# Performance work log

Hardware: AMD Instinct MI355X
Metric: run time of the kernel (lower is better)

## Reference

```python
import jax, jax.numpy as jnp
import numpy as np

H, C, HID, NLAYERS, B = 4, 32, 128, 3, 2048
EPS = 1e-5


def _gat_layer(x, src, dst, n, W, b, a_src, a_dst):
    # x: [N, HID]; W: [HID, H*C]; a_src/a_dst: [H, C]
    h = (x @ W).reshape(n, H, C)                      # [N,H,C]
    s_src = jnp.einsum('nhc,hc->nh', h, a_src)        # [N,H]
    s_dst = jnp.einsum('nhc,hc->nh', h, a_dst)
    e = jax.nn.leaky_relu(s_src[src] + s_dst[dst], 0.2)   # [E,H]
    m = jax.ops.segment_max(e, dst, num_segments=n)
    p = jnp.exp(e - m[dst])
    z = jax.ops.segment_sum(p, dst, num_segments=n)
    alpha = p / z[dst]                                 # scatter-softmax over in-edges
    msg = h[src] * alpha[:, :, None]                   # [E,H,C]
    out = jax.ops.segment_sum(msg, dst, num_segments=n)
    return out.reshape(n, H * C) + b


def _layernorm(x, g, bta):
    mu = jnp.mean(x, axis=-1, keepdims=True)
    var = jnp.mean(jnp.square(x - mu), axis=-1, keepdims=True)
    return (x - mu) * jax.lax.rsqrt(var + EPS) * g + bta


def _encode(x, edge_index, batch, W_in, b_in, Wg, bg, att_src, att_dst, ln_gamma, ln_beta):
    n = x.shape[0]
    # add self loops (PyG GATConv default)
    loops = jnp.arange(n, dtype=edge_index.dtype)
    src = jnp.concatenate([edge_index[0], loops])
    dst = jnp.concatenate([edge_index[1], loops])
    h = jax.nn.relu(x @ W_in + b_in)
    for i in range(NLAYERS):
        res = h
        h = _gat_layer(h, src, dst, n, Wg[i], bg[i], att_src[i], att_dst[i])
        h = _layernorm(h, ln_gamma[i], ln_beta[i])
        h = jax.nn.relu(h)
        h = h + res
    # global mean pool
    sums = jax.ops.segment_sum(h, batch, num_segments=B)
    cnt = jax.ops.segment_sum(jnp.ones((n,), h.dtype), batch, num_segments=B)
    return sums / jnp.maximum(cnt, 1.0)[:, None]


def setup_inputs() -> dict:
    key = jax.random.key(0)
    ks = jax.random.split(key, 24)
    Nt, Et, Np, Ep, D = 131072, 2097152, 24576, 196608, 480
    inp = {}
    inp['tcr_x'] = jax.random.normal(ks[0], (Nt, D), jnp.float32)
    inp['tcr_edge_index'] = jax.random.randint(ks[1], (2, Et), 0, Nt)
    inp['tcr_batch'] = jnp.sort(jax.random.randint(ks[2], (Nt,), 0, B))
    inp['pep_x'] = jax.random.normal(ks[3], (Np, D), jnp.float32)
    inp['pep_edge_index'] = jax.random.randint(ks[4], (2, Ep), 0, Np)
    inp['pep_batch'] = jnp.sort(jax.random.randint(ks[5], (Np,), 0, B))
    s_in = 1.0 / np.sqrt(D)
    inp['W_in'] = jax.random.normal(ks[6], (D, HID), jnp.float32) * s_in
    inp['b_in'] = jnp.zeros((HID,), jnp.float32)
    s_h = 1.0 / np.sqrt(HID)
    inp['Wg'] = jax.random.normal(ks[7], (NLAYERS, HID, H * C), jnp.float32) * s_h
    inp['bg'] = jnp.zeros((NLAYERS, HID), jnp.float32)
    inp['att_src'] = jax.random.normal(ks[8], (NLAYERS, H, C), jnp.float32) * (1.0 / np.sqrt(C))
    inp['att_dst'] = jax.random.normal(ks[9], (NLAYERS, H, C), jnp.float32) * (1.0 / np.sqrt(C))
    inp['ln_gamma'] = jnp.ones((NLAYERS, HID), jnp.float32)
    inp['ln_beta'] = jnp.zeros((NLAYERS, HID), jnp.float32)
    inp['Wc1'] = jax.random.normal(ks[10], (2 * HID, HID), jnp.float32) * (1.0 / np.sqrt(2 * HID))
    inp['bc1'] = jnp.zeros((HID,), jnp.float32)
    inp['Wc2'] = jax.random.normal(ks[11], (HID, HID // 2), jnp.float32) * s_h
    inp['bc2'] = jnp.zeros((HID // 2,), jnp.float32)
    inp['Wc3'] = jax.random.normal(ks[12], (HID // 2, 1), jnp.float32) * (1.0 / np.sqrt(HID // 2))
    inp['bc3'] = jnp.zeros((1,), jnp.float32)
    return inp


def reference(tcr_x, tcr_edge_index, tcr_batch, pep_x, pep_edge_index, pep_batch,
              W_in, b_in, Wg, bg, att_src, att_dst, ln_gamma, ln_beta,
              Wc1, bc1, Wc2, bc2, Wc3, bc3):
    tcr = _encode(tcr_x, tcr_edge_index, tcr_batch, W_in, b_in, Wg, bg, att_src, att_dst, ln_gamma, ln_beta)
    pep = _encode(pep_x, pep_edge_index, pep_batch, W_in, b_in, Wg, bg, att_src, att_dst, ln_gamma, ln_beta)
    z = jnp.concatenate([tcr, pep], axis=1)            # [B, 256]
    z = jax.nn.relu(z @ Wc1 + bc1)
    z = jax.nn.relu(z @ Wc2 + bc2)
    return jax.nn.sigmoid(z @ Wc3 + bc3)               # [B, 1]
```

## Files before the change

kernel.cpp:

```cpp
#include <hip/hip_runtime.h>
#include <hip/hip_fp16.h>
#include <math.h>

#define NHEAD   4
#define CDIM    32
#define HIDDIM  128
#define NLAYERS 3
#define DIN     480
#define LN_EPS  1e-5f
#define NSPLIT  4

typedef _Float16 f16x8 __attribute__((ext_vector_type(8)));
typedef float    f32x4 __attribute__((ext_vector_type(4)));
typedef int      int4u __attribute__((ext_vector_type(4), aligned(4)));

__global__ void hist_kernel(const int* __restrict__ tei, const int* __restrict__ pei,
                            int* __restrict__ deg, int Et, int Ep, int Nt, int N) {
    int i = blockIdx.x * 256 + threadIdx.x;
    int tot = Et + Ep + N;
    if (i >= tot) return;
    int d;
    if (i < Et)            d = tei[Et + i];
    else if (i < Et + Ep)  d = pei[Ep + (i - Et)] + Nt;
    else                   d = i - Et - Ep;
    atomicAdd(&deg[d], 1);
}

__global__ __launch_bounds__(256) void fill_kernel(const int* __restrict__ tei,
                                                   const int* __restrict__ pei,
                                                   int* __restrict__ cursor,
                                                   int* __restrict__ col,
                                                   int Et, int Ep, int Nt, int N,
                                                   float oscale) {
    int oid    = blockIdx.x & (NSPLIT - 1);
    int chunk  = blockIdx.x / NSPLIT;
    int nchunk = gridDim.x / NSPLIT;
    int tot = Et + Ep + N;
    int per = (tot + nchunk - 1) / nchunk;
    int e0 = chunk * per;
    int e1 = min(e0 + per, tot);
    for (int i = e0 + (int)threadIdx.x; i < e1; i += 256) {
        int d;
        bool self = false;
        if (i < Et)           d = tei[Et + i];
        else if (i < Et + Ep) d = pei[Ep + (i - Et)] + Nt;
        else                { d = i - Et - Ep; self = true; }
        int owner = (int)((float)d * oscale);
        owner = owner > NSPLIT - 1 ? NSPLIT - 1 : owner;
        if (owner != oid) continue;
        int s;
        if (self)        s = d;
        else if (i < Et) s = tei[i];
        else             s = pei[i - Et] + Nt;
        int pos = atomicAdd(&cursor[d], 1);
        col[pos] = s;
    }
}

__global__ __launch_bounds__(256) void scan_reduce(const int* __restrict__ deg,
                                                   int* __restrict__ part, int N) {
    __shared__ int sm[256];
    int t = threadIdx.x;
    int base = blockIdx.x * 1024 + t * 4;
    int4 v = make_int4(0, 0, 0, 0);
    if (base + 3 < N) v = *(const int4*)(deg + base);
    else if (base < N) {
        v.x = deg[base];
        if (base + 1 < N) v.y = deg[base + 1];
        if (base + 2 < N) v.z = deg[base + 2];
    }
    sm[t] = v.x + v.y + v.z + v.w;
    __syncthreads();
    for (int off = 128; off >= 1; off >>= 1) {
        if (t < off) sm[t] += sm[t + off];
        __syncthreads();
    }
    if (t == 0) part[blockIdx.x] = sm[0];
}

__global__ __launch_bounds__(256) void scan_partials(int* __restrict__ part,
                                                     int* __restrict__ rowptr,
                                                     int npart, int N) {
    __shared__ int sm[256];
    int t = threadIdx.x;
    sm[t] = (t < npart) ? part[t] : 0;
    __syncthreads();
    for (int off = 1; off < 256; off <<= 1) {
        int u = (t >= off) ? sm[t - off] : 0;
        __syncthreads();
        sm[t] += u;
        __syncthreads();
    }
    if (t < npart) part[t] = (t == 0) ? 0 : sm[t - 1];
    if (t == 0) rowptr[N] = sm[255];
}

__global__ __launch_bounds__(256) void scan_final(const int* __restrict__ deg,
                                                  const int* __restrict__ part,
                                                  int* __restrict__ rowptr,
                                                  int* __restrict__ cursor, int N) {
    __shared__ int sm[256];
    int t = threadIdx.x;
    int base = blockIdx.x * 1024 + t * 4;
    int4 v = make_int4(0, 0, 0, 0);
    if (base + 3 < N) v = *(const int4*)(deg + base);
    else if (base < N) {
        v.x = deg[base];
        if (base + 1 < N) v.y = deg[base + 1];
        if (base + 2 < N) v.z = deg[base + 2];
    }
    sm[t] = v.x + v.y + v.z + v.w;
    __syncthreads();
    for (int off = 1; off < 256; off <<= 1) {
        int u = (t >= off) ? sm[t - off] : 0;
        __syncthreads();
        sm[t] += u;
        __syncthreads();
    }
    int run = ((t == 0) ? 0 : sm[t - 1]) + part[blockIdx.x];
    if (base < N)     { rowptr[base]     = run; cursor[base]     = run; run += v.x; }
    if (base + 1 < N) { rowptr[base + 1] = run; cursor[base + 1] = run; run += v.y; }
    if (base + 2 < N) { rowptr[base + 2] = run; cursor[base + 2] = run; run += v.z; }
    if (base + 3 < N) { rowptr[base + 3] = run; cursor[base + 3] = run; }
}

__global__ void transpose_w(const float* __restrict__ W, _Float16* __restrict__ Wt,
                            int K) {
    int idx = blockIdx.x * 256 + threadIdx.x;
    if (idx >= K * 128) return;
    int n = idx / K, k = idx - n * K;
    Wt[idx] = (_Float16)W[(size_t)k * 128 + n];
}

#define ASTRIDE 40

template<int OUT_F16>
__global__ __launch_bounds__(256) void mfma_gemm(const float* __restrict__ A,
                                                 const _Float16* __restrict__ Wt,
                                                 const float* __restrict__ bias,
                                                 void* __restrict__ Cout,
                                                 int K) {
    __shared__ _Float16 As[64 * ASTRIDE];
    __shared__ _Float16 Ws[128 * ASTRIDE];
    const int tid  = threadIdx.x;
    const int bn   = blockIdx.x * 64;
    const int wave = tid >> 6, lane = tid & 63;
    const int lm   = lane & 15, q = lane >> 4;

    f32x4 acc[8];
#pragma unroll
    for (int i = 0; i < 8; ++i) acc[i] = (f32x4){0.f, 0.f, 0.f, 0.f};

    for (int kt = 0; kt < K; kt += 32) {
#pragma unroll
        for (int p = 0; p < 2; ++p) {
            int f  = p * 256 + tid;
            int r  = f >> 3;
            int c4 = (f & 7) * 4;
            float4 v = *(const float4*)(A + (size_t)(bn + r) * K + kt + c4);
            _Float16* d = &As[r * ASTRIDE + c4];
            d[0] = (_Float16)v.x; d[1] = (_Float16)v.y;
            d[2] = (_Float16)v.z; d[3] = (_Float16)v.w;
        }
#pragma unroll
        for (int p = 0; p < 2; ++p) {
            int f   = p * 256 + tid;
            int n   = f >> 2;
            int seg = (f & 3) * 8;
            *(float4*)(&Ws[n * ASTRIDE + seg]) =
                *(const float4*)(Wt + (size_t)n * K + kt + seg);
        }
        __syncthreads();
        f16x8 af = *(const f16x8*)(&As[(wave * 16 + lm) * ASTRIDE + q * 8]);
#pragma unroll
        for (int nt = 0; nt < 8; ++nt) {
            f16x8 bf = *(const f16x8*)(&Ws[(nt * 16 + lm) * ASTRIDE + q * 8]);
            acc[nt] = __builtin_amdgcn_mfma_f32_16x16x32_f16(af, bf, acc[nt], 0, 0, 0);
        }
        __syncthreads();
    }

    const int row0 = bn + wave * 16 + q * 4;
    if (OUT_F16) {
        _Float16* C = (_Float16*)Cout;
#pragma unroll
        for (int nt = 0; nt < 8; ++nt) {
            int c = nt * 16 + lm;
#pragma unroll
            for (int i = 0; i < 4; ++i)
                C[(size_t)(row0 + i) * 128 + c] = (_Float16)acc[nt][i];
        }
    } else {
        float* C = (float*)Cout;
#pragma unroll
        for (int nt = 0; nt < 8; ++nt) {
            int c = nt * 16 + lm;
            float bv = bias[c];
#pragma unroll
            for (int i = 0; i < 4; ++i)
                C[(size_t)(row0 + i) * 128 + c] = fmaxf(acc[nt][i] + bv, 0.f);
        }
    }
}

__global__ __launch_bounds__(256) void scores_kernel(const __half2* __restrict__ h2v,
                                                     const float* __restrict__ a_src,
                                                     const float* __restrict__ a_dst,
                                                     float* __restrict__ ssrc,
                                                     float* __restrict__ sdst, int N) {
    int wave = threadIdx.x >> 6, lane = threadIdx.x & 63;
    int n = blockIdx.x * 4 + wave;
    if (n >= N) return;
    int c = lane * 2, h = lane >> 4, t = lane & 15;
    float2 v = __half22float2(h2v[(size_t)n * 64 + lane]);
    float2 as = *(const float2*)(a_src + c);
    float2 ad = *(const float2*)(a_dst + c);
    float ps = v.x * as.x + v.y * as.y;
    float pd = v.x * ad.x + v.y * ad.y;
#pragma unroll
    for (int k = 1; k < 16; k <<= 1) {
        ps += __shfl_xor(ps, k, 16);
        pd += __shfl_xor(pd, k, 16);
    }
    if (t == 0) {
        ssrc[n * 4 + h] = ps;
        sdst[n * 4 + h] = pd;
    }
}

__global__ __launch_bounds__(256) void gather_kernel(const f16x8* __restrict__ h2v,
                                                     const float* __restrict__ ssrc,
                                                     const float* __restrict__ sdst,
                                                     const int* __restrict__ rowptr,
                                                     const int* __restrict__ col,
                                                     const float* __restrict__ bg,
                                                     const float* __restrict__ gamma,
                                                     const float* __restrict__ beta,
                                                     float* __restrict__ hio, int N) {
    int wave = threadIdx.x >> 6, lane = threadIdx.x & 63;
    int g = lane >> 4, t = lane & 15;
    int n = blockIdx.x * 16 + wave * 4 + g;
    bool valid = n < N;
    int nn = valid ? n : 0;
    int head = t >> 2;
    int beg = rowptr[nn];
    int end = valid ? rowptr[nn + 1] : beg;
    float sd = sdst[nn * 4 + head];

    float m = -1e30f, z = 0.f;
    float a[8];
#pragma unroll
    for (int k = 0; k < 8; ++k) a[k] = 0.f;

    int j = beg;
    for (; j + 3 < end; j += 4) {
        int4u cv = *(const int4u*)(col + j);
        int s0 = cv.x, s1 = cv.y, s2 = cv.z, s3 = cv.w;
        float e0 = ssrc[s0 * 4 + head] + sd;
        float e1 = ssrc[s1 * 4 + head] + sd;
        float e2 = ssrc[s2 * 4 + head] + sd;
        float e3 = ssrc[s3 * 4 + head] + sd;
        f16x8 v0 = h2v[(size_t)s0 * 16 + t];
        f16x8 v1 = h2v[(size_t)s1 * 16 + t];
        f16x8 v2 = h2v[(size_t)s2 * 16 + t];
        f16x8 v3 = h2v[(size_t)s3 * 16 + t];
        e0 = fmaxf(e0, 0.2f * e0);
        e1 = fmaxf(e1, 0.2f * e1);
        e2 = fmaxf(e2, 0.2f * e2);
        e3 = fmaxf(e3, 0.2f * e3);
        float nm = fmaxf(fmaxf(fmaxf(e0, e1), fmaxf(e2, e3)), m);
        float r  = __expf(m - nm);
        m = nm;
        float p0 = __expf(e0 - nm);
        float p1 = __expf(e1 - nm);
        float p2 = __expf(e2 - nm);
        float p3 = __expf(e3 - nm);
        z = z * r + (p0 + p1 + p2 + p3);
#pragma unroll
        for (int k = 0; k < 8; ++k) a[k] *= r;
#pragma unroll
        for (int k = 0; k < 8; ++k) a[k] = fmaf((float)v0[k], p0, a[k]);
#pragma unroll
        for (int k = 0; k < 8; ++k) a[k] = fmaf((float)v1[k], p1, a[k]);
#pragma unroll
        for (int k = 0; k < 8; ++k) a[k] = fmaf((float)v2[k], p2, a[k]);
#pragma unroll
        for (int k = 0; k < 8; ++k) a[k] = fmaf((float)v3[k], p3, a[k]);
    }
    for (; j < end; ++j) {
        int s = col[j];
        float e = ssrc[s * 4 + head] + sd;
        e = fmaxf(e, 0.2f * e);
        f16x8 v = h2v[(size_t)s * 16 + t];
        float nm = fmaxf(m, e);
        float r  = __expf(m - nm);
        float p  = __expf(e - nm);
        m = nm;
        z = z * r + p;
#pragma unroll
        for (int k = 0; k < 8; ++k) a[k] = fmaf((float)v[k], p, a[k] * r);
    }

    if (!valid) return;
    float inv = 1.f / z;
    int c0 = t * 8;
    float4 bgv0 = *(const float4*)(bg + c0);
    float4 bgv1 = *(const float4*)(bg + c0 + 4);
    float o[8];
    o[0] = a[0] * inv + bgv0.x; o[1] = a[1] * inv + bgv0.y;
    o[2] = a[2] * inv + bgv0.z; o[3] = a[3] * inv + bgv0.w;
    o[4] = a[4] * inv + bgv1.x; o[5] = a[5] * inv + bgv1.y;
    o[6] = a[6] * inv + bgv1.z; o[7] = a[7] * inv + bgv1.w;
    float s = 0.f;
#pragma unroll
    for (int k = 0; k < 8; ++k) s += o[k];
#pragma unroll
    for (int k = 1; k < 16; k <<= 1) s += __shfl_xor(s, k, 16);
    float mu = s * (1.f / 128.f);
    float q = 0.f;
#pragma unroll
    for (int k = 0; k < 8; ++k) q += (o[k] - mu) * (o[k] - mu);
#pragma unroll
    for (int k = 1; k < 16; k <<= 1) q += __shfl_xor(q, k, 16);
    float rs = rsqrtf(q * (1.f / 128.f) + LN_EPS);
    float4 gm0 = *(const float4*)(gamma + c0);
    float4 gm1 = *(const float4*)(gamma + c0 + 4);
    float4 bt0 = *(const float4*)(beta + c0);
    float4 bt1 = *(const float4*)(beta + c0 + 4);
    float* hrow = hio + (size_t)n * 128 + c0;
    float4 r0 = *(const float4*)(hrow);
    float4 r1 = *(const float4*)(hrow + 4);
    float4 y0, y1;
    y0.x = fmaxf((o[0] - mu) * rs * gm0.x + bt0.x, 0.f) + r0.x;
    y0.y = fmaxf((o[1] - mu) * rs * gm0.y + bt0.y, 0.f) + r0.y;
    y0.z = fmaxf((o[2] - mu) * rs * gm0.z + bt0.z, 0.f) + r0.z;
    y0.w = fmaxf((o[3] - mu) * rs * gm0.w + bt0.w, 0.f) + r0.w;
    y1.x = fmaxf((o[4] - mu) * rs * gm1.x + bt1.x, 0.f) + r1.x;
    y1.y = fmaxf((o[5] - mu) * rs * gm1.y + bt1.y, 0.f) + r1.y;
    y1.z = fmaxf((o[6] - mu) * rs * gm1.z + bt1.z, 0.f) + r1.z;
    y1.w = fmaxf((o[7] - mu) * rs * gm1.w + bt1.w, 0.f) + r1.w;
    *(float4*)(hrow)     = y0;
    *(float4*)(hrow + 4) = y1;
}

__global__ __launch_bounds__(256) void pool_kernel(const float* __restrict__ h,
                                                   const int* __restrict__ tb,
                                                   const int* __restrict__ pb,
                                                   float* __restrict__ pooled,
                                                   int* __restrict__ cnt,
                                                   int Nt, int N, int B) {
    int wave = threadIdx.x >> 6, lane = threadIdx.x & 63;
    int n = blockIdx.x * 4 + wave;
    if (n >= N) return;
    int b, off, ci;
    if (n < Nt) { b = tb[n];      off = 0;   ci = b; }
    else        { b = pb[n - Nt]; off = 128; ci = B + b; }
    float v0 = h[(size_t)n * 128 + lane];
    float v1 = h[(size_t)n * 128 + 64 + lane];
    atomicAdd(&pooled[(size_t)b * 256 + off + lane], v0);
    atomicAdd(&pooled[(size_t)b * 256 + off + 64 + lane], v1);
    if (lane == 0) atomicAdd(&cnt[ci], 1);
}

__global__ __launch_bounds__(128) void classifier_kernel(const float* __restrict__ pooled,
                                                         const int* __restrict__ cnt,
                                                         const float* __restrict__ Wc1,
                                                         const float* __restrict__ bc1,
                                                         const float* __restrict__ Wc2,
                                                         const float* __restrict__ bc2,
                                                         const float* __restrict__ Wc3,
                                                         const float* __restrict__ bc3,
                                                         float* __restrict__ outp, int B) {
    __shared__ float z[256];
    __shared__ float a1[128];
    __shared__ float a2[64];
    int r = blockIdx.x, t = threadIdx.x;
    float ct = (float)max(cnt[r], 1);
    float cp = (float)max(cnt[B + r], 1);
    z[t]       = pooled[(size_t)r * 256 + t] / ct;
    z[128 + t] = pooled[(size_t)r * 256 + 128 + t] / cp;
    __syncthreads();
    float acc = bc1[t];
    for (int k = 0; k < 256; ++k) acc = fmaf(z[k], Wc1[k * 128 + t], acc);
    a1[t] = fmaxf(acc, 0.f);
    __syncthreads();
    if (t < 64) {
        float a = bc2[t];
        for (int k = 0; k < 128; ++k) a = fmaf(a1[k], Wc2[k * 64 + t], a);
        a2[t] = fmaxf(a, 0.f);
    }
    __syncthreads();
    if (t < 64) {
        float p = a2[t] * Wc3[t];
#pragma unroll
        for (int k = 1; k < 64; k <<= 1) p += __shfl_xor(p, k);
        if (t == 0) outp[r] = 1.f / (1.f + __expf(-(p + bc3[0])));
    }
}

extern "C" void kernel_launch(void* const* d_in, const int* in_sizes, int n_in,
                              void* d_out, int out_size, void* d_ws, size_t ws_size,
                              hipStream_t stream) {
    const float* tcr_x     = (const float*)d_in[0];
    const int*   tcr_ei    = (const int*)d_in[1];
    const int*   tcr_batch = (const int*)d_in[2];
    const float* pep_x     = (const float*)d_in[3];
    const int*   pep_ei    = (const int*)d_in[4];
    const int*   pep_batch = (const int*)d_in[5];
    const float* W_in      = (const float*)d_in[6];
    const float* b_in      = (const float*)d_in[7];
    const float* Wg        = (const float*)d_in[8];
    const float* bg        = (const float*)d_in[9];
    const float* att_src   = (const float*)d_in[10];
    const float* att_dst   = (const float*)d_in[11];
    const float* ln_gamma  = (const float*)d_in[12];
    const float* ln_beta   = (const float*)d_in[13];
    const float* Wc1       = (const float*)d_in[14];
    const float* bc1       = (const float*)d_in[15];
    const float* Wc2       = (const float*)d_in[16];
    const float* bc2       = (const float*)d_in[17];
    const float* Wc3       = (const float*)d_in[18];
    const float* bc3       = (const float*)d_in[19];

    const int Nt = in_sizes[0] / DIN;
    const int Et = in_sizes[1] / 2;
    const int Np = in_sizes[3] / DIN;
    const int Ep = in_sizes[4] / 2;
    const int B  = out_size;
    const int N  = Nt + Np;
    const int Etot = Et + Ep + N;

    char* w = (char*)d_ws;
    size_t o = 0;
    auto alloc = [&](size_t bytes) -> char* {
        size_t r = (o + 255) & ~(size_t)255;
        o = r + bytes;
        return w + r;
    };
    float*    pooled = (float*)alloc((size_t)B * 256 * 4);
    int*      cnt    = (int*)alloc((size_t)B * 2 * 4);
    float*    h_a    = (float*)alloc((size_t)N * 128 * 4);
    _Float16* h2h    = (_Float16*)alloc((size_t)N * 128 * 2);
    _Float16* WtIn   = (_Float16*)alloc((size_t)128 * DIN * 2);
    _Float16* WtG    = (_Float16*)alloc((size_t)NLAYERS * 128 * 128 * 2);
    float*    ssrc   = (float*)alloc((size_t)N * 4 * 4);
    float*    sdst   = (float*)alloc((size_t)N * 4 * 4);
    int* rowptr      = (int*)alloc((size_t)(N + 1) * 4);
    int* cursor      = (int*)alloc((size_t)N * 4);
    int* deg         = (int*)alloc((size_t)N * 4);
    int* part        = (int*)alloc(256 * 4);
    int* col         = (int*)alloc((size_t)Etot * 4);
    (void)ws_size; (void)n_in;

    hipMemsetAsync(pooled, 0, (size_t)B * 256 * 4, stream);
    hipMemsetAsync(cnt, 0, (size_t)B * 2 * 4, stream);
    hipMemsetAsync(deg, 0, (size_t)N * 4, stream);

    transpose_w<<<(128 * DIN + 255) / 256, 256, 0, stream>>>(W_in, WtIn, DIN);
    for (int i = 0; i < NLAYERS; ++i)
        transpose_w<<<(128 * 128 + 255) / 256, 256, 0, stream>>>(
            Wg + (size_t)i * HIDDIM * HIDDIM, WtG + (size_t)i * 128 * 128, 128);

    hist_kernel<<<(Etot + 255) / 256, 256, 0, stream>>>(tcr_ei, pep_ei, deg, Et, Ep, Nt, N);
    int nblk = (N + 1023) / 1024;
    scan_reduce<<<nblk, 256, 0, stream>>>(deg, part, N);
    scan_partials<<<1, 256, 0, stream>>>(part, rowptr, nblk, N);
    scan_final<<<nblk, 256, 0, stream>>>(deg, part, rowptr, cursor, N);
    fill_kernel<<<NSPLIT * 512, 256, 0, stream>>>(tcr_ei, pep_ei, cursor, col,
                                                  Et, Ep, Nt, N, (float)NSPLIT / (float)N);

    mfma_gemm<0><<<Nt / 64, 256, 0, stream>>>(tcr_x, WtIn, b_in, h_a, DIN);
    mfma_gemm<0><<<Np / 64, 256, 0, stream>>>(pep_x, WtIn, b_in, h_a + (size_t)Nt * 128, DIN);

    for (int i = 0; i < NLAYERS; ++i) {
        mfma_gemm<1><<<N / 64, 256, 0, stream>>>(h_a, WtG + (size_t)i * 128 * 128,
                                                 nullptr, h2h, 128);
        scores_kernel<<<(N + 3) / 4, 256, 0, stream>>>((const __half2*)h2h,
                                                       att_src + i * NHEAD * CDIM,
                                                       att_dst + i * NHEAD * CDIM,
                                                       ssrc, sdst, N);
        gather_kernel<<<(N + 15) / 16, 256, 0, stream>>>((const f16x8*)h2h, ssrc, sdst,
                                                         rowptr, col, bg + i * HIDDIM,
                                                         ln_gamma + i * HIDDIM,
                                                         ln_beta + i * HIDDIM, h_a, N);
    }
    pool_kernel<<<(N + 3) / 4, 256, 0, stream>>>(h_a, tcr_batch, pep_batch, pooled, cnt, Nt, N, B);

    classifier_kernel<<<B, 128, 0, stream>>>(pooled, cnt, Wc1, bc1, Wc2, bc2,
                                             Wc3, bc3, (float*)d_out, B);
}
```

Before: 1.293 ms.

## Fuse attention scores into GEMM epilogue and segment-based mean pooling

Computes the per-head source and destination attention scores inside the f16 GEMM epilogue using shuffle reductions over the accumulator fragments. This removes the separate scores kernel and its re-read of h2h. Pooling now uses one block per graph, finding the node range by binary search on the sorted batch arrays and dividing by the count directly. That drops the atomics, the count buffer and two memsets, but it depends on the batch arrays being sorted.

```diff
diff --git a/kernel.cpp b/kernel.cpp
--- a/kernel.cpp
+++ b/kernel.cpp
@@ -139,6 +139,10 @@
                                                  const _Float16* __restrict__ Wt,
                                                  const float* __restrict__ bias,
                                                  void* __restrict__ Cout,
+                                                 const float* __restrict__ a_src,
+                                                 const float* __restrict__ a_dst,
+                                                 float* __restrict__ ssrc,
+                                                 float* __restrict__ sdst,
                                                  int K) {
     __shared__ _Float16 As[64 * ASTRIDE];
     __shared__ _Float16 Ws[128 * ASTRIDE];
@@ -183,13 +187,37 @@
     const int row0 = bn + wave * 16 + q * 4;
     if (OUT_F16) {
         _Float16* C = (_Float16*)Cout;
+        float as[8], ad[8];
 #pragma unroll
         for (int nt = 0; nt < 8; ++nt) {
-            int c = nt * 16 + lm;
-#pragma unroll
-            for (int i = 0; i < 4; ++i)
-                C[(size_t)(row0 + i) * 128 + c] = (_Float16)acc[nt][i];
+            as[nt] = a_src[nt * 16 + lm];
+            ad[nt] = a_dst[nt * 16 + lm];
         }
+        float myS = 0.f, myD = 0.f;
+#pragma unroll
+        for (int i = 0; i < 4; ++i) {
+            float ps[4], pd[4];
+#pragma unroll
+            for (int h = 0; h < 4; ++h) {
+                ps[h] = as[2 * h] * acc[2 * h][i] + as[2 * h + 1] * acc[2 * h + 1][i];
+                pd[h] = ad[2 * h] * acc[2 * h][i] + ad[2 * h + 1] * acc[2 * h + 1][i];
+            }
+#pragma unroll
+            for (int k = 1; k < 16; k <<= 1) {
+#pragma unroll
+                for (int h = 0; h < 4; ++h) {
+                    ps[h] += __shfl_xor(ps[h], k, 16);
+                    pd[h] += __shfl_xor(pd[h], k, 16);
+                }
+            }
+            if ((lm >> 2) == i) { myS = ps[lm & 3]; myD = pd[lm & 3]; }
+#pragma unroll
+            for (int nt = 0; nt < 8; ++nt)
+                C[(size_t)(row0 + i) * 128 + nt * 16 + lm] = (_Float16)acc[nt][i];
+        }
+        int sr = (row0 + (lm >> 2)) * 4 + (lm & 3);
+        ssrc[sr] = myS;
+        sdst[sr] = myD;
     } else {
         float* C = (float*)Cout;
 #pragma unroll
@@ -200,31 +228,6 @@
             for (int i = 0; i < 4; ++i)
                 C[(size_t)(row0 + i) * 128 + c] = fmaxf(acc[nt][i] + bv, 0.f);
         }
-    }
-}
-
-__global__ __launch_bounds__(256) void scores_kernel(const __half2* __restrict__ h2v,
-                                                     const float* __restrict__ a_src,
-                                                     const float* __restrict__ a_dst,
-                                                     float* __restrict__ ssrc,
-                                                     float* __restrict__ sdst, int N) {
-    int wave = threadIdx.x >> 6, lane = threadIdx.x & 63;
-    int n = blockIdx.x * 4 + wave;
-    if (n >= N) return;
-    int c = lane * 2, h = lane >> 4, t = lane & 15;
-    float2 v = __half22float2(h2v[(size_t)n * 64 + lane]);
-    float2 as = *(const float2*)(a_src + c);
-    float2 ad = *(const float2*)(a_dst + c);
-    float ps = v.x * as.x + v.y * as.y;
-    float pd = v.x * ad.x + v.y * ad.y;
-#pragma unroll
-    for (int k = 1; k < 16; k <<= 1) {
-        ps += __shfl_xor(ps, k, 16);
-        pd += __shfl_xor(pd, k, 16);
-    }
-    if (t == 0) {
-        ssrc[n * 4 + h] = ps;
-        sdst[n * 4 + h] = pd;
     }
 }
 
@@ -343,27 +346,40 @@
     *(float4*)(hrow + 4) = y1;
 }
 
-__global__ __launch_bounds__(256) void pool_kernel(const float* __restrict__ h,
+__global__ __launch_bounds__(128) void pool_kernel(const float* __restrict__ h,
                                                    const int* __restrict__ tb,
                                                    const int* __restrict__ pb,
                                                    float* __restrict__ pooled,
-                                                   int* __restrict__ cnt,
-                                                   int Nt, int N, int B) {
-    int wave = threadIdx.x >> 6, lane = threadIdx.x & 63;
-    int n = blockIdx.x * 4 + wave;
-    if (n >= N) return;
-    int b, off, ci;
-    if (n < Nt) { b = tb[n];      off = 0;   ci = b; }
-    else        { b = pb[n - Nt]; off = 128; ci = B + b; }
-    float v0 = h[(size_t)n * 128 + lane];
-    float v1 = h[(size_t)n * 128 + 64 + lane];
-    atomicAdd(&pooled[(size_t)b * 256 + off + lane], v0);
-    atomicAdd(&pooled[(size_t)b * 256 + off + 64 + lane], v1);
-    if (lane == 0) atomicAdd(&cnt[ci], 1);
+                                                   int Nt, int Np, int B) {
+    int blk = blockIdx.x;
+    bool is_t = blk < B;
+    int bb = is_t ? blk : blk - B;
+    const int* __restrict__ arr = is_t ? tb : pb;
+    int len  = is_t ? Nt : Np;
+    int base = is_t ? 0 : Nt;
+    int off  = is_t ? 0 : 128;
+    int lo = 0, hi = len;
+    while (lo < hi) { int mid = (lo + hi) >> 1; if (arr[mid] < bb) lo = mid + 1; else hi = mid; }
+    int beg = lo;
+    hi = len;
+    while (lo < hi) { int mid = (lo + hi) >> 1; if (arr[mid] < bb + 1) lo = mid + 1; else hi = mid; }
+    int end = lo;
+    int t = threadIdx.x;
+    float a0 = 0.f, a1 = 0.f, a2 = 0.f, a3 = 0.f;
+    int n = beg;
+    for (; n + 3 < end; n += 4) {
+        a0 += h[(size_t)(base + n)     * 128 + t];
+        a1 += h[(size_t)(base + n + 1) * 128 + t];
+        a2 += h[(size_t)(base + n + 2) * 128 + t];
+        a3 += h[(size_t)(base + n + 3) * 128 + t];
+    }
+    for (; n < end; ++n) a0 += h[(size_t)(base + n) * 128 + t];
+    float s = (a0 + a1) + (a2 + a3);
+    float invc = 1.f / (float)max(end - beg, 1);
+    pooled[(size_t)bb * 256 + off + t] = s * invc;
 }
 
 __global__ __launch_bounds__(128) void classifier_kernel(const float* __restrict__ pooled,
-                                                         const int* __restrict__ cnt,
                                                          const float* __restrict__ Wc1,
                                                          const float* __restrict__ bc1,
                                                          const float* __restrict__ Wc2,
@@ -375,10 +391,8 @@
     __shared__ float a1[128];
     __shared__ float a2[64];
     int r = blockIdx.x, t = threadIdx.x;
-    float ct = (float)max(cnt[r], 1);
-    float cp = (float)max(cnt[B + r], 1);
-    z[t]       = pooled[(size_t)r * 256 + t] / ct;
-    z[128 + t] = pooled[(size_t)r * 256 + 128 + t] / cp;
+    z[t]       = pooled[(size_t)r * 256 + t];
+    z[128 + t] = pooled[(size_t)r * 256 + 128 + t];
     __syncthreads();
     float acc = bc1[t];
     for (int k = 0; k < 256; ++k) acc = fmaf(z[k], Wc1[k * 128 + t], acc);
@@ -438,7 +452,6 @@
         return w + r;
     };
     float*    pooled = (float*)alloc((size_t)B * 256 * 4);
-    int*      cnt    = (int*)alloc((size_t)B * 2 * 4);
     float*    h_a    = (float*)alloc((size_t)N * 128 * 4);
     _Float16* h2h    = (_Float16*)alloc((size_t)N * 128 * 2);
     _Float16* WtIn   = (_Float16*)alloc((size_t)128 * DIN * 2);
@@ -452,8 +465,6 @@
     int* col         = (int*)alloc((size_t)Etot * 4);
     (void)ws_size; (void)n_in;
 
-    hipMemsetAsync(pooled, 0, (size_t)B * 256 * 4, stream);
-    hipMemsetAsync(cnt, 0, (size_t)B * 2 * 4, stream);
     hipMemsetAsync(deg, 0, (size_t)N * 4, stream);
 
     transpose_w<<<(128 * DIN + 255) / 256, 256, 0, stream>>>(W_in, WtIn, DIN);
@@ -469,23 +480,24 @@
     fill_kernel<<<NSPLIT * 512, 256, 0, stream>>>(tcr_ei, pep_ei, cursor, col,
                                                   Et, Ep, Nt, N, (float)NSPLIT / (float)N);
 
-    mfma_gemm<0><<<Nt / 64, 256, 0, stream>>>(tcr_x, WtIn, b_in, h_a, DIN);
-    mfma_gemm<0><<<Np / 64, 256, 0, stream>>>(pep_x, WtIn, b_in, h_a + (size_t)Nt * 128, DIN);
+    mfma_gemm<0><<<Nt / 64, 256, 0, stream>>>(tcr_x, WtIn, b_in, h_a,
+                                              nullptr, nullptr, nullptr, nullptr, DIN);
+    mfma_gemm<0><<<Np / 64, 256, 0, stream>>>(pep_x, WtIn, b_in, h_a + (size_t)Nt * 128,
+                                              nullptr, nullptr, nullptr, nullptr, DIN);
 
     for (int i = 0; i < NLAYERS; ++i) {
         mfma_gemm<1><<<N / 64, 256, 0, stream>>>(h_a, WtG + (size_t)i * 128 * 128,
-                                                 nullptr, h2h, 128);
-        scores_kernel<<<(N + 3) / 4, 256, 0, stream>>>((const __half2*)h2h,
-                                                       att_src + i * NHEAD * CDIM,
-                                                       att_dst + i * NHEAD * CDIM,
-                                                       ssrc, sdst, N);
+                                                 nullptr, h2h,
+                                                 att_src + i * NHEAD * CDIM,
+                                                 att_dst + i * NHEAD * CDIM,
+                                                 ssrc, sdst, 128);
         gather_kernel<<<(N + 15) / 16, 256, 0, stream>>>((const f16x8*)h2h, ssrc, sdst,
                                                          rowptr, col, bg + i * HIDDIM,
                                                          ln_gamma + i * HIDDIM,
                                                          ln_beta + i * HIDDIM, h_a, N);
     }
-    pool_kernel<<<(N + 3) / 4, 256, 0, stream>>>(h_a, tcr_batch, pep_batch, pooled, cnt, Nt, N, B);
-
-    classifier_kernel<<<B, 128, 0, stream>>>(pooled, cnt, Wc1, bc1, Wc2, bc2,
+    pool_kernel<<<2 * B, 128, 0, stream>>>(h_a, tcr_batch, pep_batch, pooled, Nt, Np, B);
+
+    classifier_kernel<<<B, 128, 0, stream>>>(pooled, Wc1, bc1, Wc2, bc2,
                                              Wc3, bc3, (float*)d_out, B);
 }
```

Result: faster. 1.148 ms (-11.2%).
